# Kernel tuning notes

Measured on AMD Instinct MI355X. Metric: run time of the kernel, lower is better.

Reference implementation:

```python
import jax, jax.numpy as jnp
import numpy as np

B, L, D, H = 2, 2048, 2048, 16
DH = D // H
SCALE = 1.0 / float(np.sqrt(DH))


def setup_inputs() -> dict:
    key = jax.random.key(0)
    ks = jax.random.split(key, 5)
    std = 1.0 / float(np.sqrt(D))
    return {
        "x": jax.random.normal(ks[0], (B, L, D), dtype=jnp.float32),
        "W_q": jax.random.normal(ks[1], (D, D), dtype=jnp.float32) * std,
        "W_k": jax.random.normal(ks[2], (D, D), dtype=jnp.float32) * std,
        "W_v": jax.random.normal(ks[3], (D, D), dtype=jnp.float32) * std,
        "W_o": jax.random.normal(ks[4], (D, D), dtype=jnp.float32) * std,
    }


def _split_heads(t):
    # (B, L, D) -> (B, H, L, DH)
    b, l, _ = t.shape
    return t.reshape(b, l, H, DH).transpose(0, 2, 1, 3)


def reference(x, W_q, W_k, W_v, W_o):
    # nn.Linear(bias=False): y = x @ W.T
    q = _split_heads(x @ W_q.T)  # (B,H,L,DH)
    k = _split_heads(x @ W_k.T)
    v = _split_heads(x @ W_v.T)
    scores = jnp.einsum("bhqd,bhkd->bhqk", q, k) * SCALE  # (B,H,L,L)
    causal = jnp.arange(L)[:, None] >= jnp.arange(L)[None, :]  # True = keep
    scores = jnp.where(causal[None, None], scores, -jnp.inf)
    attn = jax.nn.softmax(scores, axis=-1)
    y = jnp.einsum("bhqk,bhkd->bhqd", attn, v)  # (B,H,L,DH)
    y = y.transpose(0, 2, 1, 3).reshape(B, L, D)  # merge heads
    return y @ W_o.T
```

## Files before the change

### kernel.cpp

```cpp
#include <hip/hip_runtime.h>
#include <hip/hip_bf16.h>
#include <stdint.h>

typedef unsigned short u16;
typedef __bf16 bf16x8 __attribute__((ext_vector_type(8)));
typedef float f32x4 __attribute__((ext_vector_type(4)));

#define SEQ    2048
#define DMODEL 2048
#define NHEAD  16
#define DHEAD  128
#define QSCALE (0.088388347648318447f * 1.4426950408889634f)

__device__ __forceinline__ u16 f2bf(float f){
  uint32_t u = __float_as_uint(f);
  u += 0x7FFFu + ((u >> 16) & 1u);
  return (u16)(u >> 16);
}

__device__ __forceinline__ void gload_lds16(const u16* g, u16* l){
  __builtin_amdgcn_global_load_lds((const __attribute__((address_space(1))) void*)g,
                                   (__attribute__((address_space(3))) void*)l,
                                   16, 0, 0);
}

__global__ __launch_bounds__(256) void cvt_all(const float* __restrict__ x,
    const float* __restrict__ Wq, const float* __restrict__ Wk,
    const float* __restrict__ Wv, const float* __restrict__ Wo,
    u16* __restrict__ dst){
  int gid = blockIdx.x * 256 + threadIdx.x;
  const float* s; int idx;
  if (gid < 2097152){ s = x; idx = gid; }
  else {
    int j = gid - 2097152;
    int z = j >> 20; idx = j & 0xFFFFF;
    s = (z==0) ? Wq : (z==1) ? Wk : (z==2) ? Wv : Wo;
  }
  float4 v = reinterpret_cast<const float4*>(s)[idx];
  ushort4 o;
  o.x = f2bf(v.x); o.y = f2bf(v.y); o.z = f2bf(v.z); o.w = f2bf(v.w);
  reinterpret_cast<ushort4*>(dst)[gid] = o;
}

__device__ __forceinline__ void stageA(const u16* __restrict__ G, int grow0, int kt,
                                       int half, u16* lds, int w, int lane){
  #pragma unroll
  for (int j = 0; j < 2; ++j){
    int q   = w*2 + j;
    int r0  = ((q & 8) << 4) + half*64 + (q & 7)*8;
    int row = r0 + (lane >> 3);
    int sc  = (lane & 7) ^ (row & 7);
    gload_lds16(G + (size_t)(grow0 + row)*DMODEL + kt*64 + sc*8, lds + r0*64);
  }
}
__device__ __forceinline__ void stageB(const u16* __restrict__ G, int grow0, int kt,
                                       int half, u16* lds, int w, int lane){
  #pragma unroll
  for (int j = 0; j < 2; ++j){
    int q   = w*2 + j;
    int r0  = ((q >> 2) << 6) + half*32 + (q & 3)*8;
    int row = r0 + (lane >> 3);
    int sc  = (lane & 7) ^ (row & 7);
    gload_lds16(G + (size_t)(grow0 + row)*DMODEL + kt*64 + sc*8, lds + r0*64);
  }
}

__device__ __forceinline__ bf16x8 ldsf(const u16* lds, int row, int c){
  return *reinterpret_cast<const bf16x8*>(lds + row*64 + (((c ^ (row & 7)) & 7) << 3));
}

template<int MH>
__device__ __forceinline__ void load_a(bf16x8 (&a)[4][2], const u16* LA,
                                       int wr, int ln, int g){
  #pragma unroll
  for (int m = 0; m < 4; ++m){
    int row = wr*128 + MH*64 + m*16 + ln;
    a[m][0] = ldsf(LA, row, g);
    a[m][1] = ldsf(LA, row, 4 + g);
  }
}
template<int NH>
__device__ __forceinline__ void load_b(bf16x8 (&b)[2][2], const u16* LB,
                                       int wc, int ln, int g){
  #pragma unroll
  for (int n = 0; n < 2; ++n){
    int row = wc*64 + NH*32 + n*16 + ln;
    b[n][0] = ldsf(LB, row, g);
    b[n][1] = ldsf(LB, row, 4 + g);
  }
}

template<int MH, int NH>
__device__ __forceinline__ void mfma_quad(f32x4 (&acc)[8][4], bf16x8 (&a)[4][2],
                                          bf16x8 (&b)[2][2]){
  __builtin_amdgcn_s_setprio(1);
  #pragma unroll
  for (int m = 0; m < 4; ++m)
    #pragma unroll
    for (int n = 0; n < 2; ++n){
      acc[MH*4+m][NH*2+n] = __builtin_amdgcn_mfma_f32_16x16x32_bf16(
          a[m][0], b[n][0], acc[MH*4+m][NH*2+n], 0, 0, 0);
      acc[MH*4+m][NH*2+n] = __builtin_amdgcn_mfma_f32_16x16x32_bf16(
          a[m][1], b[n][1], acc[MH*4+m][NH*2+n], 0, 0, 0);
    }
  __builtin_amdgcn_s_setprio(0);
}

__device__ __forceinline__ void phase_pre(){
  __builtin_amdgcn_s_barrier();
  asm volatile("s_waitcnt lgkmcnt(0)" ::: "memory");
  __builtin_amdgcn_sched_barrier(0);
}

__device__ __forceinline__ void gemm8_core(const u16* __restrict__ A,
    const u16* __restrict__ W, int bm, int bnl,
    u16 (*ldsA)[256*64], u16 (*ldsB)[256*64], f32x4 (&acc)[8][4],
    int w, int lane, int wr, int wc, int g, int ln){
  const f32x4 z4 = {0.f,0.f,0.f,0.f};
  #pragma unroll
  for (int i = 0; i < 8; ++i)
    #pragma unroll
    for (int j = 0; j < 4; ++j) acc[i][j] = z4;

  stageA(A, bm, 0, 0, ldsA[0], w, lane);
  stageB(W, bnl, 0, 1, ldsB[0], w, lane);
  stageA(A, bm, 0, 1, ldsA[0], w, lane);
  stageB(W, bnl, 0, 0, ldsB[0], w, lane);
  stageA(A, bm, 1, 0, ldsA[1], w, lane);
  stageB(W, bnl, 1, 1, ldsB[1], w, lane);
  asm volatile("s_waitcnt vmcnt(4)" ::: "memory");
  __builtin_amdgcn_s_barrier();

  bf16x8 a[4][2], b[2][2];
  const int NT = DMODEL/64;
  for (int t = 0; t < NT; ++t){
    const int cur = t & 1;
    const u16* LA = ldsA[cur];
    const u16* LB = ldsB[cur];
    load_a<0>(a, LA, wr, ln, g);
    load_b<0>(b, LB, wc, ln, g);
    if (t+1 < NT) stageA(A, bm, t+1, 1, ldsA[cur^1], w, lane);
    phase_pre();
    mfma_quad<0,0>(acc, a, b);
    __builtin_amdgcn_s_barrier();
    load_b<1>(b, LB, wc, ln, g);
    if (t+1 < NT) stageB(W, bnl, t+1, 0, ldsB[cur^1], w, lane);
    phase_pre();
    mfma_quad<0,1>(acc, a, b);
    __builtin_amdgcn_s_barrier();
    load_a<1>(a, LA, wr, ln, g);
    if (t+2 < NT) stageA(A, bm, t+2, 0, ldsA[cur], w, lane);
    phase_pre();
    mfma_quad<1,1>(acc, a, b);
    __builtin_amdgcn_s_barrier();
    load_b<0>(b, LB, wc, ln, g);
    if (t+2 < NT) stageB(W, bnl, t+2, 1, ldsB[cur], w, lane);
    if (t < NT-2) { asm volatile("s_waitcnt vmcnt(4)" ::: "memory"); }
    else          { asm volatile("s_waitcnt vmcnt(0)" ::: "memory"); }
    phase_pre();
    mfma_quad<1,0>(acc, a, b);
    __builtin_amdgcn_s_barrier();
  }
}

__global__ __launch_bounds__(512, 2) void gemm_qkv8(const u16* __restrict__ A,
    const u16* __restrict__ Wall, u16* __restrict__ Q, u16* __restrict__ Kb,
    u16* __restrict__ Vt){
  __shared__ __align__(16) u16 ldsA[2][256*64];
  __shared__ __align__(16) u16 ldsB[2][256*64];
  const int tid = threadIdx.x, w = tid >> 6, lane = tid & 63;
  const int g = lane >> 4, ln = lane & 15;
  const int wr = w >> 2, wc = w & 3;
  const int bid = blockIdx.x;
  const int swz = (bid & 7)*48 + (bid >> 3);
  const int nt = swz >> 4, mt = swz & 15;
  const int bm = mt*256, z = nt >> 3, bnl = (nt & 7) << 8;
  const u16* W = Wall + ((size_t)z << 22);
  f32x4 acc[8][4];
  gemm8_core(A, W, bm, bnl, ldsA, ldsB, acc, w, lane, wr, wc, g, ln);

  if (z < 2){
    u16* C = (z == 0) ? Q : Kb;
    const float sc = (z == 0) ? QSCALE : 1.0f;
    #pragma unroll
    for (int mf = 0; mf < 8; ++mf)
      #pragma unroll
      for (int nf = 0; nf < 4; ++nf){
        int col = bnl + wc*64 + nf*16 + ln;
        #pragma unroll
        for (int i = 0; i < 4; ++i){
          int row = bm + wr*128 + mf*16 + g*4 + i;
          C[(size_t)row*DMODEL + col] = f2bf(acc[mf][nf][i] * sc);
        }
      }
  } else {
    #pragma unroll
    for (int mf = 0; mf < 8; ++mf)
      #pragma unroll
      for (int nf = 0; nf < 4; ++nf){
        int col  = bnl + wc*64 + nf*16 + ln;
        int row0 = bm + wr*128 + mf*16 + g*4;
        int bb   = row0 >> 11, lt = row0 & (SEQ-1);
        ushort4 pk;
        pk.x = f2bf(acc[mf][nf][0]); pk.y = f2bf(acc[mf][nf][1]);
        pk.z = f2bf(acc[mf][nf][2]); pk.w = f2bf(acc[mf][nf][3]);
        *reinterpret_cast<ushort4*>(Vt + (size_t)(bb*DMODEL + col)*SEQ + lt) = pk;
      }
  }
}

__device__ __forceinline__ void stageB3(const u16* __restrict__ G, int grow0,
    int kt, u16* lds, int w, int lane){
  #pragma unroll
  for (int j = 0; j < 2; ++j){
    int q   = w*2 + j;
    int r0  = q*8;
    int row = r0 + (lane >> 3);
    int sc  = (lane & 7) ^ (row & 7);
    gload_lds16(G + (size_t)(grow0 + row)*DMODEL + kt*64 + sc*8, lds + r0*64);
  }
}

__device__ __forceinline__ void load_b3(bf16x8 (&b)[2][2], const u16* LB,
                                        int wc, int ln, int g){
  #pragma unroll
  for (int n = 0; n < 2; ++n){
    int row = wc*32 + n*16 + ln;
    b[n][0] = ldsf(LB, row, g);
    b[n][1] = ldsf(LB, row, 4 + g);
  }
}

template<int MH>
__device__ __forceinline__ void mfma8x2(f32x4 (&acc)[8][2], bf16x8 (&a)[4][2],
                                        bf16x8 (&b)[2][2]){
  __builtin_amdgcn_s_setprio(1);
  #pragma unroll
  for (int m = 0; m < 4; ++m)
    #pragma unroll
    for (int n = 0; n < 2; ++n){
      acc[MH*4+m][n] = __builtin_amdgcn_mfma_f32_16x16x32_bf16(
          a[m][0], b[n][0], acc[MH*4+m][n], 0, 0, 0);
      acc[MH*4+m][n] = __builtin_amdgcn_mfma_f32_16x16x32_bf16(
          a[m][1], b[n][1], acc[MH*4+m][n], 0, 0, 0);
    }
  __builtin_amdgcn_s_setprio(0);
}

__global__ __launch_bounds__(512, 2) void gemm_out3(const u16* __restrict__ A,
    const u16* __restrict__ Wo, float* __restrict__ C){
  __shared__ __align__(16) u16 ldsA[2][256*64];
  __shared__ __align__(16) u16 ldsB[2][128*64];
  const int tid = threadIdx.x, w = tid >> 6, lane = tid & 63;
  const int g = lane >> 4, ln = lane & 15;
  const int wr = w >> 2, wc = w & 3;
  const int bid = blockIdx.x;
  const int x = bid & 7, s = bid >> 3;
  const int mt = s >> 1, nt = 2*x + (s & 1);
  const int bm = mt*256, bnl = nt << 7;
  f32x4 acc[8][2];
  {
    const f32x4 z4 = {0.f,0.f,0.f,0.f};
    #pragma unroll
    for (int i = 0; i < 8; ++i){ acc[i][0] = z4; acc[i][1] = z4; }
  }
  stageA (A,  bm,  0, 0, ldsA[0], w, lane);
  stageA (A,  bm,  0, 1, ldsA[0], w, lane);
  stageB3(Wo, bnl, 0,    ldsB[0], w, lane);
  stageA (A,  bm,  1, 0, ldsA[1], w, lane);
  asm volatile("s_waitcnt vmcnt(2)" ::: "memory");
  __builtin_amdgcn_s_barrier();

  bf16x8 a[4][2], b[2][2];
  const int NT = DMODEL/64;
  for (int t = 0; t < NT; ++t){
    const int cur = t & 1;
    const u16* LA = ldsA[cur];
    const u16* LB = ldsB[cur];
    load_a<0>(a, LA, wr, ln, g);
    load_b3(b, LB, wc, ln, g);
    if (t+1 < NT){
      stageA (A,  bm,  t+1, 1, ldsA[cur^1], w, lane);
      stageB3(Wo, bnl, t+1,    ldsB[cur^1], w, lane);
    }
    phase_pre();
    mfma8x2<0>(acc, a, b);
    __builtin_amdgcn_s_barrier();
    load_a<1>(a, LA, wr, ln, g);
    if (t+2 < NT) stageA(A, bm, t+2, 0, ldsA[cur], w, lane);
    if (t < NT-2) { asm volatile("s_waitcnt vmcnt(2)" ::: "memory"); }
    else          { asm volatile("s_waitcnt vmcnt(0)" ::: "memory"); }
    phase_pre();
    mfma8x2<1>(acc, a, b);
    __builtin_amdgcn_s_barrier();
  }

  #pragma unroll
  for (int mf = 0; mf < 8; ++mf)
    #pragma unroll
    for (int nf = 0; nf < 2; ++nf){
      int col = bnl + wc*32 + nf*16 + ln;
      #pragma unroll
      for (int i = 0; i < 4; ++i){
        int row = bm + wr*128 + mf*16 + g*4 + i;
        C[(size_t)row*DMODEL + col] = acc[mf][nf][i];
      }
    }
}

__device__ __forceinline__ void attn_stageK(const u16* __restrict__ Kb,
    u16* Kt, int b, int h, int kb, int w, int lane){
  #pragma unroll
  for (int is = 0; is < 4; ++is){
    int o = w*4096 + is*1024 + lane*16;
    int row = o >> 8;
    int sc  = ((o >> 4) & 15) ^ (row & 7);
    gload_lds16(Kb + (size_t)(b*SEQ + kb + row)*DMODEL + h*DHEAD + sc*8,
                Kt + w*2048 + is*512);
  }
}
__device__ __forceinline__ void attn_stageV(const u16* __restrict__ Vtb,
    u16* Vt, int bh, int kb, int w, int lane){
  #pragma unroll
  for (int is = 0; is < 4; ++is){
    int o = w*4096 + is*1024 + lane*16;
    int row = o >> 7;
    int sc  = ((o >> 4) & 7) ^ (row & 7);
    gload_lds16(Vtb + (size_t)(bh*DHEAD + row)*SEQ + kb + sc*8,
                Vt + w*2048 + is*512);
  }
}

template<bool MASKED>
__device__ __forceinline__ void attn_qkt_sm(const u16* Kt, u16* Pw,
    const bf16x8 (&qf)[2][4], f32x4 (&yacc)[2][8],
    float (&mrun)[2], float (&lrun)[2],
    int kb, int qg0, int g, int ln){
  #pragma unroll
  for (int qc = 0; qc < 2; ++qc){
    f32x4 st[4];
    __builtin_amdgcn_s_setprio(1);
    #pragma unroll
    for (int kt = 0; kt < 4; ++kt){
      f32x4 accs = {0.f,0.f,0.f,0.f};
      #pragma unroll
      for (int c = 0; c < 4; ++c){
        int row = kt*16 + ln;
        int ch  = (c*4 + g) ^ (row & 7);
        bf16x8 kf = *reinterpret_cast<const bf16x8*>(Kt + row*128 + ch*8);
        accs = __builtin_amdgcn_mfma_f32_16x16x32_bf16(kf, qf[qc][c], accs, 0, 0, 0);
      }
      st[kt] = accs;
    }
    __builtin_amdgcn_s_setprio(0);

    const int qg = qg0 + qc*16;
    float p[16];
    float tmax = -1e30f;
    #pragma unroll
    for (int kt = 0; kt < 4; ++kt)
      #pragma unroll
      for (int i = 0; i < 4; ++i){
        float s = st[kt][i];
        if (MASKED && (kb + kt*16 + g*4 + i) > qg) s = -1e30f;
        p[kt*4+i] = s;
        tmax = fmaxf(tmax, s);
      }
    tmax = fmaxf(tmax, __shfl_xor(tmax, 16));
    tmax = fmaxf(tmax, __shfl_xor(tmax, 32));

    if (!__all(tmax - mrun[qc] <= 11.5f)){
      float mn = fmaxf(mrun[qc], tmax);
      float fr = __builtin_amdgcn_exp2f(mrun[qc] - mn);
      lrun[qc] *= fr;
      float fi[4];
      #pragma unroll
      for (int i = 0; i < 4; ++i) fi[i] = __shfl(fr, g*4 + i);
      #pragma unroll
      for (int dt = 0; dt < 8; ++dt)
        #pragma unroll
        for (int i = 0; i < 4; ++i) yacc[qc][dt][i] *= fi[i];
      mrun[qc] = mn;
    }
    float psum = 0.f;
    #pragma unroll
    for (int j = 0; j < 16; ++j){
      p[j] = __builtin_amdgcn_exp2f(p[j] - mrun[qc]);
      psum += p[j];
    }
    psum += __shfl_xor(psum, 16);
    psum += __shfl_xor(psum, 32);
    lrun[qc] += psum;

    char* pb = reinterpret_cast<char*>(Pw + qc*1024);
    #pragma unroll
    for (int kt = 0; kt < 4; ++kt)
      #pragma unroll
      for (int pr = 0; pr < 2; ++pr){
        uint32_t pk = (uint32_t)f2bf(p[kt*4 + 2*pr]) |
                      ((uint32_t)f2bf(p[kt*4 + 2*pr + 1]) << 16);
        int byte = (kt*16 + g*4 + 2*pr)*2;
        int ch   = (byte >> 4) ^ (ln & 7);
        int addr = ln*128 + (ch << 4) + (byte & 15);
        *reinterpret_cast<uint32_t*>(pb + addr) = pk;
      }
  }
}

__device__ __forceinline__ void attn_pv(const u16* Vt, const u16* Pw,
                                        f32x4 (&yacc)[2][8], int g, int ln){
  __builtin_amdgcn_s_setprio(1);
  #pragma unroll
  for (int kc = 0; kc < 2; ++kc){
    int chp = (kc*4 + g) ^ (ln & 7);
    bf16x8 pf0 = *reinterpret_cast<const bf16x8*>(Pw +        ln*64 + chp*8);
    bf16x8 pf1 = *reinterpret_cast<const bf16x8*>(Pw + 1024 + ln*64 + chp*8);
    #pragma unroll
    for (int dt = 0; dt < 8; ++dt){
      int row = dt*16 + ln;
      int chv = (kc*4 + g) ^ (row & 7);
      bf16x8 vf = *reinterpret_cast<const bf16x8*>(Vt + row*64 + chv*8);
      yacc[0][dt] = __builtin_amdgcn_mfma_f32_16x16x32_bf16(pf0, vf, yacc[0][dt], 0, 0, 0);
      yacc[1][dt] = __builtin_amdgcn_mfma_f32_16x16x32_bf16(pf1, vf, yacc[1][dt], 0, 0, 0);
    }
  }
  __builtin_amdgcn_s_setprio(0);
}

__global__ __launch_bounds__(256, 2) void attn_fwd(const u16* __restrict__ Qb,
    const u16* __restrict__ Kb, const u16* __restrict__ Vtb, u16* __restrict__ Yb){
  __shared__ __align__(16) u16 Kt[2][64*128];
  __shared__ __align__(16) u16 Vt[2][128*64];
  __shared__ __align__(16) u16 Pl[4][2048];
  const int tid = threadIdx.x, w = tid >> 6, lane = tid & 63;
  const int g = lane >> 4, ln = lane & 15;
  const int bh = blockIdx.y;
  const int b = bh >> 4, h = bh & 15;
  const int qb = (bh < 16) ? blockIdx.x : (15 - blockIdx.x);
  const int qw = qb*128 + w*32;
  const int qg0 = qw + ln;
  const int NT = 2*qb + 2;

  bf16x8 qf[2][4];
  #pragma unroll
  for (int qc = 0; qc < 2; ++qc){
    const u16* qp = Qb + (size_t)(b*SEQ + qw + qc*16 + ln)*DMODEL + h*DHEAD + g*8;
    #pragma unroll
    for (int c = 0; c < 4; ++c) qf[qc][c] = *reinterpret_cast<const bf16x8*>(qp + c*32);
  }
  float mrun[2] = {-1e30f, -1e30f}, lrun[2] = {0.f, 0.f};
  f32x4 yacc[2][8];
  {
    const f32x4 z4 = {0.f,0.f,0.f,0.f};
    #pragma unroll
    for (int qc = 0; qc < 2; ++qc)
      #pragma unroll
      for (int dt = 0; dt < 8; ++dt) yacc[qc][dt] = z4;
  }
  u16* Pw = &Pl[w][0];

  attn_stageK(Kb, &Kt[0][0], b, h, 0, w, lane);
  attn_stageV(Vtb, &Vt[0][0], bh, 0, w, lane);
  asm volatile("s_waitcnt vmcnt(0)" ::: "memory");
  __builtin_amdgcn_s_barrier();

  int cur = 0;
  for (int t = 0; t < NT; ++t){
    const int kb = t*64;
    if (t+1 < NT){
      attn_stageK(Kb, &Kt[cur^1][0], b, h, kb + 64, w, lane);
      attn_stageV(Vtb, &Vt[cur^1][0], bh, kb + 64, w, lane);
    }
    bool active = true;
    if (t < NT-2){
      attn_qkt_sm<false>(&Kt[cur][0], Pw, qf, yacc, mrun, lrun, kb, qg0, g, ln);
    } else if (t == NT-2){
      if (w >= 2) attn_qkt_sm<false>(&Kt[cur][0], Pw, qf, yacc, mrun, lrun, kb, qg0, g, ln);
      else        attn_qkt_sm<true >(&Kt[cur][0], Pw, qf, yacc, mrun, lrun, kb, qg0, g, ln);
    } else {
      if (w >= 2) attn_qkt_sm<true >(&Kt[cur][0], Pw, qf, yacc, mrun, lrun, kb, qg0, g, ln);
      else        active = false;
    }
    if (active) attn_pv(&Vt[cur][0], Pw, yacc, g, ln);
    asm volatile("s_waitcnt vmcnt(0) lgkmcnt(0)" ::: "memory");
    __builtin_amdgcn_s_barrier();
    cur ^= 1;
  }

  #pragma unroll
  for (int qc = 0; qc < 2; ++qc){
    float inv[4];
    #pragma unroll
    for (int i = 0; i < 4; ++i){
      float li = __shfl(lrun[qc], g*4 + i);
      inv[i] = __builtin_amdgcn_rcpf(li);
    }
    #pragma unroll
    for (int dt = 0; dt < 8; ++dt)
      #pragma unroll
      for (int i = 0; i < 4; ++i){
        Yb[(size_t)(b*SEQ + qw + qc*16 + g*4 + i)*DMODEL + h*DHEAD + dt*16 + ln] =
            f2bf(yacc[qc][dt][i] * inv[i]);
      }
  }
}

extern "C" void kernel_launch(void* const* d_in, const int* in_sizes, int n_in,
                              void* d_out, int out_size, void* d_ws, size_t ws_size,
                              hipStream_t stream) {
  const float* x  = (const float*)d_in[0];
  const float* Wq = (const float*)d_in[1];
  const float* Wk = (const float*)d_in[2];
  const float* Wv = (const float*)d_in[3];
  const float* Wo = (const float*)d_in[4];
  float* out = (float*)d_out;

  char* ws = (char*)d_ws;
  u16* xb  = (u16*)(ws +          0);
  u16* Wqb = (u16*)(ws + 16777216);
  u16* Wob = (u16*)(ws + 41943040);
  u16* Qb  = (u16*)(ws + 50331648);
  u16* Kb  = (u16*)(ws + 67108864);
  u16* Vtb = (u16*)(ws + 83886080);
  u16* Yb  = (u16*)(ws + 100663296);

  cvt_all<<<dim3(24576), 256, 0, stream>>>(x, Wq, Wk, Wv, Wo, xb);

  gemm_qkv8<<<dim3(384), 512, 0, stream>>>(xb, Wqb, Qb, Kb, Vtb);

  attn_fwd<<<dim3(16, 32), 256, 0, stream>>>(Qb, Kb, Vtb, Yb);

  gemm_out3<<<dim3(256), 512, 0, stream>>>(Yb, Wob, out);
}
```

Before: 276.9 us.

## Retile fused QKV GEMM to 256x192 tiles for even wave count

The fused QKV projection GEMM moves from 256x256 tiles (384 blocks, 2 per CU) to 256x192 tiles (512 blocks, 1 per CU). With 256 CUs, the new tile count gives exactly two full waves of blocks instead of a partial second wave. The inner loop drops from four MFMA phases to two, staging the full B tile in one step. Output columns are now mapped to Q, K or V per fragment, since a 192-wide tile can straddle the matrix boundaries. The cost is lower occupancy (launch bound 1 block per CU), a shallower pipeline, and less operand reuse per tile.

```diff
diff --git a/kernel.cpp b/kernel.cpp
--- a/kernel.cpp
+++ b/kernel.cpp
@@ -53,17 +53,6 @@
     gload_lds16(G + (size_t)(grow0 + row)*DMODEL + kt*64 + sc*8, lds + r0*64);
   }
 }
-__device__ __forceinline__ void stageB(const u16* __restrict__ G, int grow0, int kt,
-                                       int half, u16* lds, int w, int lane){
-  #pragma unroll
-  for (int j = 0; j < 2; ++j){
-    int q   = w*2 + j;
-    int r0  = ((q >> 2) << 6) + half*32 + (q & 3)*8;
-    int row = r0 + (lane >> 3);
-    int sc  = (lane & 7) ^ (row & 7);
-    gload_lds16(G + (size_t)(grow0 + row)*DMODEL + kt*64 + sc*8, lds + r0*64);
-  }
-}
 
 __device__ __forceinline__ bf16x8 ldsf(const u16* lds, int row, int c){
   return *reinterpret_cast<const bf16x8*>(lds + row*64 + (((c ^ (row & 7)) & 7) << 3));
@@ -79,32 +68,6 @@
     a[m][1] = ldsf(LA, row, 4 + g);
   }
 }
-template<int NH>
-__device__ __forceinline__ void load_b(bf16x8 (&b)[2][2], const u16* LB,
-                                       int wc, int ln, int g){
-  #pragma unroll
-  for (int n = 0; n < 2; ++n){
-    int row = wc*64 + NH*32 + n*16 + ln;
-    b[n][0] = ldsf(LB, row, g);
-    b[n][1] = ldsf(LB, row, 4 + g);
-  }
-}
-
-template<int MH, int NH>
-__device__ __forceinline__ void mfma_quad(f32x4 (&acc)[8][4], bf16x8 (&a)[4][2],
-                                          bf16x8 (&b)[2][2]){
-  __builtin_amdgcn_s_setprio(1);
-  #pragma unroll
-  for (int m = 0; m < 4; ++m)
-    #pragma unroll
-    for (int n = 0; n < 2; ++n){
-      acc[MH*4+m][NH*2+n] = __builtin_amdgcn_mfma_f32_16x16x32_bf16(
-          a[m][0], b[n][0], acc[MH*4+m][NH*2+n], 0, 0, 0);
-      acc[MH*4+m][NH*2+n] = __builtin_amdgcn_mfma_f32_16x16x32_bf16(
-          a[m][1], b[n][1], acc[MH*4+m][NH*2+n], 0, 0, 0);
-    }
-  __builtin_amdgcn_s_setprio(0);
-}
 
 __device__ __forceinline__ void phase_pre(){
   __builtin_amdgcn_s_barrier();
@@ -112,101 +75,119 @@
   __builtin_amdgcn_sched_barrier(0);
 }
 
-__device__ __forceinline__ void gemm8_core(const u16* __restrict__ A,
-    const u16* __restrict__ W, int bm, int bnl,
-    u16 (*ldsA)[256*64], u16 (*ldsB)[256*64], f32x4 (&acc)[8][4],
-    int w, int lane, int wr, int wc, int g, int ln){
-  const f32x4 z4 = {0.f,0.f,0.f,0.f};
-  #pragma unroll
-  for (int i = 0; i < 8; ++i)
-    #pragma unroll
-    for (int j = 0; j < 4; ++j) acc[i][j] = z4;
-
-  stageA(A, bm, 0, 0, ldsA[0], w, lane);
-  stageB(W, bnl, 0, 1, ldsB[0], w, lane);
-  stageA(A, bm, 0, 1, ldsA[0], w, lane);
-  stageB(W, bnl, 0, 0, ldsB[0], w, lane);
-  stageA(A, bm, 1, 0, ldsA[1], w, lane);
-  stageB(W, bnl, 1, 1, ldsB[1], w, lane);
-  asm volatile("s_waitcnt vmcnt(4)" ::: "memory");
+__device__ __forceinline__ void stageB192(const u16* __restrict__ G, int grow0,
+    int kt, u16* lds, int w, int lane){
+  #pragma unroll
+  for (int j = 0; j < 3; ++j){
+    int q   = w*3 + j;
+    int r0  = q*8;
+    int row = r0 + (lane >> 3);
+    int sc  = (lane & 7) ^ (row & 7);
+    gload_lds16(G + (size_t)(grow0 + row)*DMODEL + kt*64 + sc*8, lds + r0*64);
+  }
+}
+
+__device__ __forceinline__ void load_b192(bf16x8 (&b)[3][2], const u16* LB,
+                                          int wc, int ln, int g){
+  #pragma unroll
+  for (int n = 0; n < 3; ++n){
+    int row = wc*48 + n*16 + ln;
+    b[n][0] = ldsf(LB, row, g);
+    b[n][1] = ldsf(LB, row, 4 + g);
+  }
+}
+
+template<int MH>
+__device__ __forceinline__ void mfma8x3(f32x4 (&acc)[8][3], bf16x8 (&a)[4][2],
+                                        bf16x8 (&b)[3][2]){
+  __builtin_amdgcn_s_setprio(1);
+  #pragma unroll
+  for (int m = 0; m < 4; ++m)
+    #pragma unroll
+    for (int n = 0; n < 3; ++n){
+      acc[MH*4+m][n] = __builtin_amdgcn_mfma_f32_16x16x32_bf16(
+          a[m][0], b[n][0], acc[MH*4+m][n], 0, 0, 0);
+      acc[MH*4+m][n] = __builtin_amdgcn_mfma_f32_16x16x32_bf16(
+          a[m][1], b[n][1], acc[MH*4+m][n], 0, 0, 0);
+    }
+  __builtin_amdgcn_s_setprio(0);
+}
+
+__global__ __launch_bounds__(512, 1) void gemm_qkv192(const u16* __restrict__ A,
+    const u16* __restrict__ Wall, u16* __restrict__ Q, u16* __restrict__ Kb,
+    u16* __restrict__ Vt){
+  __shared__ __align__(16) u16 ldsA[2][256*64];
+  __shared__ __align__(16) u16 ldsB[2][192*64];
+  const int tid = threadIdx.x, w = tid >> 6, lane = tid & 63;
+  const int g = lane >> 4, ln = lane & 15;
+  const int wr = w >> 2, wc = w & 3;
+  const int bid = blockIdx.x;
+  const int swz = (bid & 7)*64 + (bid >> 3);
+  const int nt = swz >> 4, mt = swz & 15;
+  const int bm = mt*256, bnl = nt*192;
+  f32x4 acc[8][3];
+  {
+    const f32x4 z4 = {0.f,0.f,0.f,0.f};
+    #pragma unroll
+    for (int i = 0; i < 8; ++i)
+      #pragma unroll
+      for (int j = 0; j < 3; ++j) acc[i][j] = z4;
+  }
+  stageA  (A,    bm,  0, 0, ldsA[0], w, lane);
+  stageA  (A,    bm,  0, 1, ldsA[0], w, lane);
+  stageB192(Wall, bnl, 0,    ldsB[0], w, lane);
+  stageA  (A,    bm,  1, 0, ldsA[1], w, lane);
+  asm volatile("s_waitcnt vmcnt(2)" ::: "memory");
   __builtin_amdgcn_s_barrier();
 
-  bf16x8 a[4][2], b[2][2];
+  bf16x8 a[4][2], b[3][2];
   const int NT = DMODEL/64;
   for (int t = 0; t < NT; ++t){
     const int cur = t & 1;
     const u16* LA = ldsA[cur];
     const u16* LB = ldsB[cur];
     load_a<0>(a, LA, wr, ln, g);
-    load_b<0>(b, LB, wc, ln, g);
-    if (t+1 < NT) stageA(A, bm, t+1, 1, ldsA[cur^1], w, lane);
+    load_b192(b, LB, wc, ln, g);
+    if (t+1 < NT){
+      stageA  (A,    bm,  t+1, 1, ldsA[cur^1], w, lane);
+      stageB192(Wall, bnl, t+1,    ldsB[cur^1], w, lane);
+    }
     phase_pre();
-    mfma_quad<0,0>(acc, a, b);
-    __builtin_amdgcn_s_barrier();
-    load_b<1>(b, LB, wc, ln, g);
-    if (t+1 < NT) stageB(W, bnl, t+1, 0, ldsB[cur^1], w, lane);
-    phase_pre();
-    mfma_quad<0,1>(acc, a, b);
+    mfma8x3<0>(acc, a, b);
     __builtin_amdgcn_s_barrier();
     load_a<1>(a, LA, wr, ln, g);
     if (t+2 < NT) stageA(A, bm, t+2, 0, ldsA[cur], w, lane);
-    phase_pre();
-    mfma_quad<1,1>(acc, a, b);
-    __builtin_amdgcn_s_barrier();
-    load_b<0>(b, LB, wc, ln, g);
-    if (t+2 < NT) stageB(W, bnl, t+2, 1, ldsB[cur], w, lane);
-    if (t < NT-2) { asm volatile("s_waitcnt vmcnt(4)" ::: "memory"); }
+    if (t < NT-2) { asm volatile("s_waitcnt vmcnt(2)" ::: "memory"); }
     else          { asm volatile("s_waitcnt vmcnt(0)" ::: "memory"); }
     phase_pre();
-    mfma_quad<1,0>(acc, a, b);
+    mfma8x3<1>(acc, a, b);
     __builtin_amdgcn_s_barrier();
   }
-}
-
-__global__ __launch_bounds__(512, 2) void gemm_qkv8(const u16* __restrict__ A,
-    const u16* __restrict__ Wall, u16* __restrict__ Q, u16* __restrict__ Kb,
-    u16* __restrict__ Vt){
-  __shared__ __align__(16) u16 ldsA[2][256*64];
-  __shared__ __align__(16) u16 ldsB[2][256*64];
-  const int tid = threadIdx.x, w = tid >> 6, lane = tid & 63;
-  const int g = lane >> 4, ln = lane & 15;
-  const int wr = w >> 2, wc = w & 3;
-  const int bid = blockIdx.x;
-  const int swz = (bid & 7)*48 + (bid >> 3);
-  const int nt = swz >> 4, mt = swz & 15;
-  const int bm = mt*256, z = nt >> 3, bnl = (nt & 7) << 8;
-  const u16* W = Wall + ((size_t)z << 22);
-  f32x4 acc[8][4];
-  gemm8_core(A, W, bm, bnl, ldsA, ldsB, acc, w, lane, wr, wc, g, ln);
-
-  if (z < 2){
-    u16* C = (z == 0) ? Q : Kb;
-    const float sc = (z == 0) ? QSCALE : 1.0f;
-    #pragma unroll
-    for (int mf = 0; mf < 8; ++mf)
-      #pragma unroll
-      for (int nf = 0; nf < 4; ++nf){
-        int col = bnl + wc*64 + nf*16 + ln;
+
+  #pragma unroll
+  for (int mf = 0; mf < 8; ++mf)
+    #pragma unroll
+    for (int nf = 0; nf < 3; ++nf){
+      int col = bnl + wc*48 + nf*16 + ln;
+      int z   = col >> 11;
+      int c2  = col & 2047;
+      if (z < 2){
+        u16* C = (z == 0) ? Q : Kb;
+        const float sc = (z == 0) ? QSCALE : 1.0f;
         #pragma unroll
         for (int i = 0; i < 4; ++i){
           int row = bm + wr*128 + mf*16 + g*4 + i;
-          C[(size_t)row*DMODEL + col] = f2bf(acc[mf][nf][i] * sc);
+          C[(size_t)row*DMODEL + c2] = f2bf(acc[mf][nf][i] * sc);
         }
-      }
-  } else {
-    #pragma unroll
-    for (int mf = 0; mf < 8; ++mf)
-      #pragma unroll
-      for (int nf = 0; nf < 4; ++nf){
-        int col  = bnl + wc*64 + nf*16 + ln;
+      } else {
         int row0 = bm + wr*128 + mf*16 + g*4;
         int bb   = row0 >> 11, lt = row0 & (SEQ-1);
         ushort4 pk;
         pk.x = f2bf(acc[mf][nf][0]); pk.y = f2bf(acc[mf][nf][1]);
         pk.z = f2bf(acc[mf][nf][2]); pk.w = f2bf(acc[mf][nf][3]);
-        *reinterpret_cast<ushort4*>(Vt + (size_t)(bb*DMODEL + col)*SEQ + lt) = pk;
+        *reinterpret_cast<ushort4*>(Vt + (size_t)(bb*DMODEL + c2)*SEQ + lt) = pk;
       }
-  }
+    }
 }
 
 __device__ __forceinline__ void stageB3(const u16* __restrict__ G, int grow0,
@@ -526,7 +507,7 @@
 
   cvt_all<<<dim3(24576), 256, 0, stream>>>(x, Wq, Wk, Wv, Wo, xb);
 
-  gemm_qkv8<<<dim3(384), 512, 0, stream>>>(xb, Wqb, Qb, Kb, Vtb);
+  gemm_qkv192<<<dim3(512), 512, 0, stream>>>(xb, Wqb, Qb, Kb, Vtb);
 
   attn_fwd<<<dim3(16, 32), 256, 0, stream>>>(Qb, Kb, Vtb, Yb);
 
```

Result: faster. 251.3 us (-9.2%).
